# Optimization experiments

Hardware: AMD Instinct MI355X
Metric: run time of the kernel (lower is better)

The kernel has to match this reference:

```python
import jax, jax.numpy as jnp
import numpy as np

B, T, D_IN, D_H1, D_H2, K = 8, 1024, 256, 1024, 1024, 9
EPS = 1e-12

def setup_inputs() -> dict:
    key = jax.random.key(0)
    ks = jax.random.split(key, 11)
    return {
        "x": jax.random.normal(ks[0], (B, T, D_IN), jnp.float32),
        "d_w": jax.random.normal(ks[1], (B, D_H1, 1, K), jnp.float32),
        "d_g": jax.random.uniform(ks[2], (B, D_H1), jnp.float32),
        "d_b": jax.random.normal(ks[3], (B, D_H1), jnp.float32) * 0.02,
        "p_w": jax.random.normal(ks[4], (B, D_H1, D_H2, 1), jnp.float32),
        "p_g": jax.random.uniform(ks[5], (B, D_H1), jnp.float32),
        "p_b": jax.random.normal(ks[6], (B, D_H2), jnp.float32) * 0.02,
        "w1_w": jax.random.normal(ks[7], (D_H1, D_IN), jnp.float32) / np.sqrt(D_IN),
        "w1_b": jnp.zeros((D_H1,), jnp.float32),
        "w2_w": jax.random.normal(ks[8], (D_IN, D_H2), jnp.float32) / np.sqrt(D_H2),
        "w2_b": jnp.zeros((D_IN,), jnp.float32),
    }

def _mish(v):
    return v * jnp.tanh(jax.nn.softplus(v))

def _wnorm(w, g):
    # F.normalize over channel dim 1, scaled by per-(batch,channel) gain g
    n = jnp.maximum(jnp.linalg.norm(w, axis=1, keepdims=True), EPS)
    return (w / n) * g[:, :, None, None]

def reference(x, d_w, d_g, d_b, p_w, p_g, p_b, w1_w, w1_b, w2_w, w2_b):
    residual = x
    # w_1: conv1x1 projection d_in -> d_hid1, channels-first [B, C, T]
    h = jnp.einsum('bti,ci->bct', x, w1_w) + w1_b[None, :, None]
    h = _mish(h)  # dropout is identity in eval
    k = d_w.shape[-1]
    p = (k - 1) // 2
    t = h.shape[-1]
    hp = jnp.pad(h, ((0, 0), (0, 0), (p, p)))
    # unfold: overlapping windows [B, C, T, K] (small fixed K loop)
    x_unf = jnp.stack([hp[:, :, i:i + t] for i in range(k)], axis=-1)
    dw = _wnorm(d_w, d_g)[:, :, 0, :]  # [B, C, K]
    y = jnp.einsum('bctk,bck->bct', x_unf, dw) + d_b[:, :, None]
    pw = _wnorm(p_w, p_g)[..., 0]      # [B, C, O]
    y = jnp.einsum('bct,bco->bot', y, pw) + p_b[:, :, None]
    # w_2: conv1x1 projection d_hid2 -> d_in, back to [B, T, d_in]
    out = jnp.einsum('bot,io->bti', y, w2_w) + w2_b
    return out + residual
```

## Files before the change

kernel.cpp:

```cpp
#include <hip/hip_runtime.h>
#include <hip/hip_bf16.h>

#define B_  8
#define T_  1024
#define DI_ 256
#define C_  1024
#define O_  1024
#define KW  9
#define BT_ 8192
#define EPSF 1e-12f

typedef unsigned short u16;
typedef u16   ushort8 __attribute__((ext_vector_type(8)));
typedef u16   ushort4v __attribute__((ext_vector_type(4)));
typedef __bf16 bf16x8 __attribute__((ext_vector_type(8)));
typedef float  f32x4  __attribute__((ext_vector_type(4)));

#define GLOAD_LDS16(g, l) __builtin_amdgcn_global_load_lds( \
    (const __attribute__((address_space(1))) void*)(g),      \
    (__attribute__((address_space(3))) void*)(l), 16, 0, 0)

__device__ __forceinline__ float bf2f(u16 u) {
    union { unsigned int i; float f; } z; z.i = ((unsigned int)u) << 16; return z.f;
}
__device__ __forceinline__ u16 f2bf(float f) {
    union { float f; unsigned int i; } z; z.f = f;
    unsigned int i = z.i;
    i += 0x7FFFu + ((i >> 16) & 1u);
    return (u16)(i >> 16);
}
__device__ __forceinline__ float mishf(float v) {
    float u = __expf(v);
    float w = 1.f + u;
    return v * (1.f - 2.f / (w * w + 1.f));
}

#define PB_XB 2048
#define PB_W1 2304
#define PB_W2 2560
#define PB_DN 2568
#define PB_PT 4616

__global__ __launch_bounds__(256)
void prep_k(const float* __restrict__ x,   u16* __restrict__ xb,
            const float* __restrict__ w1w, u16* __restrict__ w1b16,
            const float* __restrict__ w2w, u16* __restrict__ w2b16,
            const float* __restrict__ d_w, const float* __restrict__ d_g,
            float* __restrict__ dwf,
            const float* __restrict__ p_w, const float* __restrict__ p_g,
            float* __restrict__ part, u16* __restrict__ pwT)
{
    const int bid = blockIdx.x;
    const int tid = threadIdx.x;

    if (bid < PB_W2) {
        const float* in;
        u16* out;
        int i;
        if (bid < PB_XB)      { in = x;   out = xb;    i = bid * 256 + tid; }
        else if (bid < PB_W1) { in = w1w; out = w1b16; i = (bid - PB_XB) * 256 + tid; }
        else                  { in = w2w; out = w2b16; i = (bid - PB_W1) * 256 + tid; }
        float4 v = ((const float4*)in)[i];
        ushort4v o;
        o.x = f2bf(v.x); o.y = f2bf(v.y); o.z = f2bf(v.z); o.w = f2bf(v.w);
        ((ushort4v*)out)[i] = o;
    } else if (bid < PB_DN) {
        __shared__ float red[KW][256];
        __shared__ float nrm[KW];
        const int b = bid - PB_W2;
        float s[KW];
#pragma unroll
        for (int k = 0; k < KW; k++) s[k] = 0.f;
        for (int c = tid; c < C_; c += 256) {
#pragma unroll
            for (int k = 0; k < KW; k++) {
                float v = d_w[((size_t)b * C_ + c) * KW + k];
                s[k] += v * v;
            }
        }
#pragma unroll
        for (int k = 0; k < KW; k++) red[k][tid] = s[k];
        __syncthreads();
        if (tid < KW) {
            float t = 0.f;
            for (int i = 0; i < 256; i++) t += red[tid][i];
            nrm[tid] = fmaxf(sqrtf(t), EPSF);
        }
        __syncthreads();
        for (int c = tid; c < C_; c += 256) {
            float g = d_g[(size_t)b * C_ + c];
#pragma unroll
            for (int k = 0; k < KW; k++)
                dwf[((size_t)b * C_ + c) * KW + k] =
                    d_w[((size_t)b * C_ + c) * KW + k] / nrm[k] * g;
        }
    } else {
        __shared__ float ts[64][65];
        __shared__ float sq[4][64];
        const int idx = bid - PB_DN;
        const int b   = idx >> 8;
        const int rem = idx & 255;
        const int c0  = (rem >> 4) * 64, o0 = (rem & 15) * 64;
        const int col = tid & 63;
        const int rg  = tid >> 6;
        float ssq = 0.f;
        for (int r = rg; r < 64; r += 4) {
            float v = p_w[((size_t)b * C_ + c0 + r) * O_ + o0 + col];
            ssq += v * v;
            ts[r][col] = v * p_g[(size_t)b * C_ + c0 + r];
        }
        sq[rg][col] = ssq;
        __syncthreads();
        if (tid < 64)
            part[((size_t)b * 16 + (rem >> 4)) * O_ + o0 + tid] =
                sq[0][tid] + sq[1][tid] + sq[2][tid] + sq[3][tid];
        for (int r = rg; r < 64; r += 4)
            pwT[((size_t)b * O_ + o0 + r) * C_ + c0 + col] = f2bf(ts[col][r]);
    }
}

__global__ __launch_bounds__(256)
void dwconv_k(const u16* __restrict__ h, const float* __restrict__ dwf,
              const float* __restrict__ d_b, u16* __restrict__ y1gT)
{
    __shared__ u16 hs[64][74];
    const int b  = blockIdx.z;
    const int c0 = blockIdx.y * 64, t0 = blockIdx.x * 64;
    const int tid = threadIdx.x;
    for (int idx = tid; idx < 64 * 72; idx += 256) {
        int cc = idx / 72, tt = idx % 72;
        int t = t0 + tt - 4;
        u16 v = 0;
        if (t >= 0 && t < T_) v = h[(size_t)(c0 + cc) * BT_ + b * T_ + t];
        hs[cc][tt] = v;
    }
    __syncthreads();
    const int cc = tid & 63;
    const int c  = c0 + cc;
    float w[KW];
#pragma unroll
    for (int k = 0; k < KW; k++) w[k] = dwf[((size_t)b * C_ + c) * KW + k];
    const float bb = d_b[(size_t)b * C_ + c];
    for (int tt = tid >> 6; tt < 64; tt += 4) {
        float s = bb;
#pragma unroll
        for (int k = 0; k < KW; k++) s += bf2f(hs[cc][tt + k]) * w[k];
        y1gT[((size_t)b * T_ + t0 + tt) * C_ + c] = f2bf(s);
    }
}

template<int EPI>
__device__ __forceinline__ void gemm12_body(
    const u16* __restrict__ A, const u16* __restrict__ Bt,
    u16* __restrict__ Db, const float* __restrict__ bias,
    const float* __restrict__ extra, int M, int N, int Kd)
{
    __shared__ u16 As[3 * 128 * 64];
    __shared__ u16 Bs[3 * 256 * 64];

    const int gx = gridDim.x;
    const unsigned nwg = (unsigned)gx * gridDim.y;
    unsigned lin = blockIdx.y * gx + blockIdx.x;
    lin = (lin & 7u) * (nwg >> 3) + (lin >> 3);
    const int m0 = (int)(lin / gx) * 128;
    const int n0 = (int)(lin % gx) * 256;

    const int b = (EPI == 1) ? (m0 >> 10) : 0;
    if (EPI == 1) {
        Bt    += (size_t)b * O_ * C_;
        bias  += (size_t)b * O_;
        extra += (size_t)b * 16 * O_;
    }

    const int tid  = threadIdx.x;
    const int lane = tid & 63, wave = tid >> 6;
    const int wm = (wave >> 2) * 64, wn = (wave & 3) * 64;
    const int lr = lane & 15;
    const int srow8 = tid >> 3;
    const int scolE = ((tid & 7) ^ ((tid >> 3) & 7)) * 8;

    f32x4 acc[4][4];
#pragma unroll
    for (int i = 0; i < 4; i++)
#pragma unroll
        for (int j = 0; j < 4; j++) acc[i][j] = (f32x4){0.f, 0.f, 0.f, 0.f};

    auto STAGE = [&](int buf, int kt) {
        const int k0 = kt << 6;
#pragma unroll
        for (int i = 0; i < 2; i++)
            GLOAD_LDS16(&A[(size_t)(m0 + i * 64 + srow8) * Kd + k0 + scolE],
                        &As[buf * 8192 + (i * 64 + wave * 8) * 64]);
#pragma unroll
        for (int i = 0; i < 4; i++)
            GLOAD_LDS16(&Bt[(size_t)(n0 + i * 64 + srow8) * Kd + k0 + scolE],
                        &Bs[buf * 16384 + (i * 64 + wave * 8) * 64]);
    };

    const int NT = Kd >> 6;
    STAGE(0, 0);
    STAGE(1, 1);
    int rb = 0, sb = 2;
    for (int kt = 0; kt < NT; kt++) {
        if (kt == NT - 1) {
            asm volatile("s_waitcnt vmcnt(0)" ::: "memory");
        } else {
            asm volatile("s_waitcnt vmcnt(6)" ::: "memory");
        }
        __builtin_amdgcn_s_barrier();
        if (kt + 2 < NT) STAGE(sb, kt + 2);
        const u16* as = &As[rb * 8192];
        const u16* bs = &Bs[rb * 16384];
        bf16x8 av[2][4], bv[2][4];
#pragma unroll
        for (int kk = 0; kk < 2; kk++) {
            const int q  = (lane >> 4) + kk * 4;
            const int sw = (q ^ (lr & 7)) << 3;
#pragma unroll
            for (int i = 0; i < 4; i++)
                av[kk][i] = *(const bf16x8*)&as[(wm + i * 16 + lr) * 64 + sw];
#pragma unroll
            for (int j = 0; j < 4; j++)
                bv[kk][j] = *(const bf16x8*)&bs[(wn + j * 16 + lr) * 64 + sw];
        }
        __builtin_amdgcn_s_setprio(1);
#pragma unroll
        for (int kk = 0; kk < 2; kk++)
#pragma unroll
            for (int i = 0; i < 4; i++)
#pragma unroll
                for (int j = 0; j < 4; j++)
                    acc[i][j] = __builtin_amdgcn_mfma_f32_16x16x32_bf16(
                        av[kk][i], bv[kk][j], acc[i][j], 0, 0, 0);
        __builtin_amdgcn_s_setprio(0);
        rb = (rb == 2) ? 0 : rb + 1;
        sb = (sb == 2) ? 0 : sb + 1;
    }

    const int r0 = (lane >> 4) * 4;
#pragma unroll
    for (int i = 0; i < 4; i++) {
#pragma unroll
        for (int j = 0; j < 4; j++) {
            const int col = n0 + wn + j * 16 + lr;
            float iv = 0.f;
            if (EPI == 1) {
                float s = 0.f;
#pragma unroll
                for (int ch = 0; ch < 16; ch++)
                    s += extra[(size_t)ch * O_ + col];
                iv = 1.f / fmaxf(sqrtf(s), EPSF);
            }
#pragma unroll
            for (int r = 0; r < 4; r++) {
                const int row = m0 + wm + i * 16 + r0 + r;
                float v = acc[i][j][r];
                if (EPI == 0) {
                    v += bias[row];
                    v = mishf(v);
                } else {
                    v = v * iv + bias[col];
                }
                Db[(size_t)row * N + col] = f2bf(v);
            }
        }
    }
}

__global__ __launch_bounds__(512, 2)
void gemm1_k(const u16* __restrict__ A, const u16* __restrict__ Bt,
             u16* __restrict__ D, const float* __restrict__ bias,
             int M, int N, int Kd)
{
    gemm12_body<0>(A, Bt, D, bias, nullptr, M, N, Kd);
}

__global__ __launch_bounds__(512, 2)
void gemm2_k(const u16* __restrict__ A, const u16* __restrict__ Bt,
             u16* __restrict__ D, const float* __restrict__ bias,
             const float* __restrict__ extra, int M, int N, int Kd)
{
    gemm12_body<1>(A, Bt, D, bias, extra, M, N, Kd);
}

__global__ __launch_bounds__(128, 2)
void gemm3_k(const u16* __restrict__ A, const u16* __restrict__ Bt,
             float* __restrict__ Df, const float* __restrict__ bias,
             const float* __restrict__ X, int M, int N, int Kd)
{
    __shared__ u16 As[3 * 2048];
    __shared__ u16 Bs[3 * 2048];

    const int gx = gridDim.x;
    const unsigned nwg = (unsigned)gx * gridDim.y;
    unsigned lin = blockIdx.y * gx + blockIdx.x;
    lin = (lin & 7u) * (nwg >> 3) + (lin >> 3);
    const int m0 = (int)(lin / gx) * 64;
    const int n0 = (int)(lin % gx) * 64;

    const int tid  = threadIdx.x;
    const int lane = tid & 63, wave = tid >> 6;
    const int wn = wave * 32;
    const int lr = lane & 15;
    const int q  = lane >> 4;
    const int srow  = lane >> 2;
    const int scolE = ((lane & 3) ^ ((lane >> 3) & 3)) * 8;
    const int sw    = (q ^ ((lr >> 1) & 3)) << 3;

    f32x4 acc[4][2];
#pragma unroll
    for (int i = 0; i < 4; i++)
#pragma unroll
        for (int j = 0; j < 2; j++) acc[i][j] = (f32x4){0.f, 0.f, 0.f, 0.f};

    auto STAGE = [&](int buf, int kt) {
        const int k0 = kt << 5;
#pragma unroll
        for (int i = 0; i < 2; i++)
            GLOAD_LDS16(&A[(size_t)(m0 + wave * 32 + i * 16 + srow) * Kd + k0 + scolE],
                        &As[buf * 2048 + (wave * 32 + i * 16) * 32]);
#pragma unroll
        for (int i = 0; i < 2; i++)
            GLOAD_LDS16(&Bt[(size_t)(n0 + wave * 32 + i * 16 + srow) * Kd + k0 + scolE],
                        &Bs[buf * 2048 + (wave * 32 + i * 16) * 32]);
    };

    const int NT = Kd >> 5;
    STAGE(0, 0);
    STAGE(1, 1);
    int rb = 0, sb = 2;
    for (int kt = 0; kt < NT; kt++) {
        if (kt == NT - 1) {
            asm volatile("s_waitcnt vmcnt(0)" ::: "memory");
        } else {
            asm volatile("s_waitcnt vmcnt(4)" ::: "memory");
        }
        __builtin_amdgcn_s_barrier();
        if (kt + 2 < NT) STAGE(sb, kt + 2);
        const u16* as = &As[rb * 2048];
        const u16* bs = &Bs[rb * 2048];
        bf16x8 av[4], bv[2];
#pragma unroll
        for (int i = 0; i < 4; i++)
            av[i] = *(const bf16x8*)&as[(i * 16 + lr) * 32 + sw];
#pragma unroll
        for (int j = 0; j < 2; j++)
            bv[j] = *(const bf16x8*)&bs[(wn + j * 16 + lr) * 32 + sw];
        __builtin_amdgcn_s_setprio(1);
#pragma unroll
        for (int i = 0; i < 4; i++)
#pragma unroll
            for (int j = 0; j < 2; j++)
                acc[i][j] = __builtin_amdgcn_mfma_f32_16x16x32_bf16(
                    av[i], bv[j], acc[i][j], 0, 0, 0);
        __builtin_amdgcn_s_setprio(0);
        rb = (rb == 2) ? 0 : rb + 1;
        sb = (sb == 2) ? 0 : sb + 1;
    }

    const int r0 = (lane >> 4) * 4;
#pragma unroll
    for (int i = 0; i < 4; i++) {
#pragma unroll
        for (int j = 0; j < 2; j++) {
            const int col = n0 + wn + j * 16 + lr;
#pragma unroll
            for (int r = 0; r < 4; r++) {
                const int row = m0 + i * 16 + r0 + r;
                Df[(size_t)row * N + col] =
                    acc[i][j][r] + bias[col] + X[(size_t)row * N + col];
            }
        }
    }
}

extern "C" void kernel_launch(void* const* d_in, const int* in_sizes, int n_in,
                              void* d_out, int out_size, void* d_ws, size_t ws_size,
                              hipStream_t stream)
{
    const float* x   = (const float*)d_in[0];
    const float* d_w = (const float*)d_in[1];
    const float* d_g = (const float*)d_in[2];
    const float* d_b = (const float*)d_in[3];
    const float* p_w = (const float*)d_in[4];
    const float* p_g = (const float*)d_in[5];
    const float* p_b = (const float*)d_in[6];
    const float* w1w = (const float*)d_in[7];
    const float* w1b = (const float*)d_in[8];
    const float* w2w = (const float*)d_in[9];
    const float* w2b = (const float*)d_in[10];
    float* out = (float*)d_out;

    char* ws = (char*)d_ws;
    const size_t SZ = (size_t)16777216;
    u16*   h    = (u16*)(ws);
    u16*   y1gT = (u16*)(ws + SZ);
    u16*   pwT  = (u16*)(ws + 2 * SZ);
    u16*   y2T  = (u16*)(ws + 3 * SZ);
    u16*   xb   = (u16*)(ws + 4 * SZ);
    u16*   w1b16= (u16*)(ws + 4 * SZ + 4194304);
    u16*   w2b16= (u16*)(ws + 4 * SZ + 4718592);
    float* dwf  = (float*)(ws + 4 * SZ + 5242880);
    float* part = (float*)(ws + 4 * SZ + 5242880 + 294912);

    prep_k<<<dim3(PB_PT), 256, 0, stream>>>(
        x, xb, w1w, w1b16, w2w, w2b16, d_w, d_g, dwf, p_w, p_g, part, pwT);

    gemm1_k<<<dim3(BT_ / 256, C_ / 128), 512, 0, stream>>>(
        w1b16, xb, h, w1b, C_, BT_, DI_);

    dwconv_k<<<dim3(T_ / 64, C_ / 64, B_), 256, 0, stream>>>(h, dwf, d_b, y1gT);

    gemm2_k<<<dim3(O_ / 256, BT_ / 128), 512, 0, stream>>>(
        y1gT, pwT, y2T, p_b, part, BT_, O_, C_);

    gemm3_k<<<dim3(DI_ / 64, BT_ / 64), 128, 0, stream>>>(
        y2T, w2b16, out, w2b, x, BT_, DI_, O_);
}
```

Baseline: 104.0 us.

## Fold pointwise and output projections into one per-batch weight matrix

Uses associativity to combine the per-batch pointwise conv weights (with their column normalization) and the final w2 projection into one [DI x C] matrix per batch, computed by a small batched GEMM. The token-sized GEMM over C->O->DI becomes a single C->DI GEMM, and the p_b bias is folded into a per-batch output bias. This removes the large intermediate y2 and most of the second big GEMM's FLOPs. The cost is an extra weight-only GEMM and an added bf16 rounding of the combined weights, which may shift numerics.

```diff
diff --git a/kernel.cpp b/kernel.cpp
--- a/kernel.cpp
+++ b/kernel.cpp
@@ -37,29 +37,29 @@
 
 #define PB_XB 2048
 #define PB_W1 2304
-#define PB_W2 2560
-#define PB_DN 2568
-#define PB_PT 4616
+#define PB_DN 2312
+#define PB_PW 2824
+#define PB_TOT 2832
 
 __global__ __launch_bounds__(256)
 void prep_k(const float* __restrict__ x,   u16* __restrict__ xb,
             const float* __restrict__ w1w, u16* __restrict__ w1b16,
-            const float* __restrict__ w2w, u16* __restrict__ w2b16,
             const float* __restrict__ d_w, const float* __restrict__ d_g,
             float* __restrict__ dwf,
             const float* __restrict__ p_w, const float* __restrict__ p_g,
-            float* __restrict__ part, u16* __restrict__ pwT)
+            u16* __restrict__ pwb, float* __restrict__ part,
+            const float* __restrict__ w2w, const float* __restrict__ p_b,
+            float* __restrict__ pb2)
 {
     const int bid = blockIdx.x;
     const int tid = threadIdx.x;
 
-    if (bid < PB_W2) {
+    if (bid < PB_W1) {
         const float* in;
         u16* out;
         int i;
-        if (bid < PB_XB)      { in = x;   out = xb;    i = bid * 256 + tid; }
-        else if (bid < PB_W1) { in = w1w; out = w1b16; i = (bid - PB_XB) * 256 + tid; }
-        else                  { in = w2w; out = w2b16; i = (bid - PB_W1) * 256 + tid; }
+        if (bid < PB_XB) { in = x;   out = xb;    i = bid * 256 + tid; }
+        else             { in = w1w; out = w1b16; i = (bid - PB_XB) * 256 + tid; }
         float4 v = ((const float4*)in)[i];
         ushort4v o;
         o.x = f2bf(v.x); o.y = f2bf(v.y); o.z = f2bf(v.z); o.w = f2bf(v.w);
@@ -67,7 +67,7 @@
     } else if (bid < PB_DN) {
         __shared__ float red[KW][256];
         __shared__ float nrm[KW];
-        const int b = bid - PB_W2;
+        const int b = bid - PB_W1;
         float s[KW];
 #pragma unroll
         for (int k = 0; k < KW; k++) s[k] = 0.f;
@@ -94,28 +94,54 @@
                 dwf[((size_t)b * C_ + c) * KW + k] =
                     d_w[((size_t)b * C_ + c) * KW + k] / nrm[k] * g;
         }
+    } else if (bid < PB_PW) {
+        const int idx = bid - PB_DN;
+        const int b   = idx >> 6;
+        const int rem = idx & 63;
+        const int cch = rem >> 2;
+        const int o   = (rem & 3) * 256 + tid;
+        float ssq = 0.f;
+#pragma unroll 8
+        for (int r = 0; r < 64; r++) {
+            const size_t row = (size_t)b * C_ + cch * 64 + r;
+            float v = p_w[row * O_ + o];
+            ssq += v * v;
+            pwb[row * O_ + o] = f2bf(v * p_g[row]);
+        }
+        part[((size_t)b * 16 + cch) * O_ + o] = ssq;
     } else {
-        __shared__ float ts[64][65];
-        __shared__ float sq[4][64];
-        const int idx = bid - PB_DN;
-        const int b   = idx >> 8;
-        const int rem = idx & 255;
-        const int c0  = (rem >> 4) * 64, o0 = (rem & 15) * 64;
-        const int col = tid & 63;
-        const int rg  = tid >> 6;
-        float ssq = 0.f;
-        for (int r = rg; r < 64; r += 4) {
-            float v = p_w[((size_t)b * C_ + c0 + r) * O_ + o0 + col];
-            ssq += v * v;
-            ts[r][col] = v * p_g[(size_t)b * C_ + c0 + r];
-        }
-        sq[rg][col] = ssq;
+        __shared__ float pbs[O_];
+        const int b = bid - PB_PW;
+        for (int j = tid; j < O_; j += 256) pbs[j] = p_b[(size_t)b * O_ + j];
         __syncthreads();
-        if (tid < 64)
-            part[((size_t)b * 16 + (rem >> 4)) * O_ + o0 + tid] =
-                sq[0][tid] + sq[1][tid] + sq[2][tid] + sq[3][tid];
-        for (int r = rg; r < 64; r += 4)
-            pwT[((size_t)b * O_ + o0 + r) * C_ + c0 + col] = f2bf(ts[col][r]);
+        const int i = tid;
+        float s = 0.f;
+        for (int o = 0; o < O_; o += 4) {
+            float4 w = *(const float4*)&w2w[(size_t)i * O_ + o];
+            s += w.x * pbs[o] + w.y * pbs[o + 1] + w.z * pbs[o + 2] + w.w * pbs[o + 3];
+        }
+        pb2[b * DI_ + i] = s;
+    }
+}
+
+__global__ __launch_bounds__(256)
+void w2s_k(const float* __restrict__ w2w, const float* __restrict__ part,
+           u16* __restrict__ w2s)
+{
+    const int bid = blockIdx.x;
+    const int tid = threadIdx.x;
+    const int b   = bid >> 4;
+    const int ich = (bid >> 2) & 3;
+    const int o   = (bid & 3) * 256 + tid;
+    float s = 0.f;
+#pragma unroll
+    for (int ch = 0; ch < 16; ch++)
+        s += part[((size_t)b * 16 + ch) * O_ + o];
+    const float inv = 1.f / fmaxf(sqrtf(s), EPSF);
+#pragma unroll 8
+    for (int r = 0; r < 64; r++) {
+        const int i = ich * 64 + r;
+        w2s[((size_t)b * DI_ + i) * O_ + o] = f2bf(w2w[(size_t)i * O_ + o] * inv);
     }
 }
 
@@ -150,10 +176,10 @@
 }
 
 template<int EPI>
-__device__ __forceinline__ void gemm12_body(
+__device__ __forceinline__ void bgemm_body(
     const u16* __restrict__ A, const u16* __restrict__ Bt,
     u16* __restrict__ Db, const float* __restrict__ bias,
-    const float* __restrict__ extra, int M, int N, int Kd)
+    int N, int Kd)
 {
     __shared__ u16 As[3 * 128 * 64];
     __shared__ u16 Bs[3 * 256 * 64];
@@ -164,13 +190,6 @@
     lin = (lin & 7u) * (nwg >> 3) + (lin >> 3);
     const int m0 = (int)(lin / gx) * 128;
     const int n0 = (int)(lin % gx) * 256;
-
-    const int b = (EPI == 1) ? (m0 >> 10) : 0;
-    if (EPI == 1) {
-        Bt    += (size_t)b * O_ * C_;
-        bias  += (size_t)b * O_;
-        extra += (size_t)b * 16 * O_;
-    }
 
     const int tid  = threadIdx.x;
     const int lane = tid & 63, wave = tid >> 6;
@@ -243,24 +262,11 @@
 #pragma unroll
         for (int j = 0; j < 4; j++) {
             const int col = n0 + wn + j * 16 + lr;
-            float iv = 0.f;
-            if (EPI == 1) {
-                float s = 0.f;
-#pragma unroll
-                for (int ch = 0; ch < 16; ch++)
-                    s += extra[(size_t)ch * O_ + col];
-                iv = 1.f / fmaxf(sqrtf(s), EPSF);
-            }
 #pragma unroll
             for (int r = 0; r < 4; r++) {
                 const int row = m0 + wm + i * 16 + r0 + r;
                 float v = acc[i][j][r];
-                if (EPI == 0) {
-                    v += bias[row];
-                    v = mishf(v);
-                } else {
-                    v = v * iv + bias[col];
-                }
+                if (EPI == 0) v = mishf(v + bias[row]);
                 Db[(size_t)row * N + col] = f2bf(v);
             }
         }
@@ -270,48 +276,52 @@
 __global__ __launch_bounds__(512, 2)
 void gemm1_k(const u16* __restrict__ A, const u16* __restrict__ Bt,
              u16* __restrict__ D, const float* __restrict__ bias,
-             int M, int N, int Kd)
-{
-    gemm12_body<0>(A, Bt, D, bias, nullptr, M, N, Kd);
+             int N, int Kd)
+{
+    bgemm_body<0>(A, Bt, D, bias, N, Kd);
 }
 
 __global__ __launch_bounds__(512, 2)
-void gemm2_k(const u16* __restrict__ A, const u16* __restrict__ Bt,
-             u16* __restrict__ D, const float* __restrict__ bias,
-             const float* __restrict__ extra, int M, int N, int Kd)
-{
-    gemm12_body<1>(A, Bt, D, bias, extra, M, N, Kd);
+void m2_k(const u16* __restrict__ A, const u16* __restrict__ Bt,
+          u16* __restrict__ D)
+{
+    const int b = blockIdx.z;
+    bgemm_body<3>(A + (size_t)b * DI_ * O_, Bt + (size_t)b * C_ * O_,
+                  D + (size_t)b * DI_ * C_, nullptr, C_, O_);
 }
 
 __global__ __launch_bounds__(128, 2)
-void gemm3_k(const u16* __restrict__ A, const u16* __restrict__ Bt,
+void fgemm_k(const u16* __restrict__ A, const u16* __restrict__ Bt,
              float* __restrict__ Df, const float* __restrict__ bias,
-             const float* __restrict__ X, int M, int N, int Kd)
+             const float* __restrict__ pb2, const float* __restrict__ X)
 {
     __shared__ u16 As[3 * 2048];
-    __shared__ u16 Bs[3 * 2048];
+    __shared__ u16 Bs[3 * 4096];
+    const int N = DI_, Kd = C_;
 
     const int gx = gridDim.x;
     const unsigned nwg = (unsigned)gx * gridDim.y;
     unsigned lin = blockIdx.y * gx + blockIdx.x;
     lin = (lin & 7u) * (nwg >> 3) + (lin >> 3);
     const int m0 = (int)(lin / gx) * 64;
-    const int n0 = (int)(lin % gx) * 64;
+    const int n0 = (int)(lin % gx) * 128;
+    const int b  = m0 >> 10;
+    const u16* Bb = Bt + (size_t)b * DI_ * C_;
 
     const int tid  = threadIdx.x;
     const int lane = tid & 63, wave = tid >> 6;
-    const int wn = wave * 32;
+    const int wn = wave * 64;
     const int lr = lane & 15;
     const int q  = lane >> 4;
     const int srow  = lane >> 2;
     const int scolE = ((lane & 3) ^ ((lane >> 3) & 3)) * 8;
     const int sw    = (q ^ ((lr >> 1) & 3)) << 3;
 
-    f32x4 acc[4][2];
+    f32x4 acc[4][4];
 #pragma unroll
     for (int i = 0; i < 4; i++)
 #pragma unroll
-        for (int j = 0; j < 2; j++) acc[i][j] = (f32x4){0.f, 0.f, 0.f, 0.f};
+        for (int j = 0; j < 4; j++) acc[i][j] = (f32x4){0.f, 0.f, 0.f, 0.f};
 
     auto STAGE = [&](int buf, int kt) {
         const int k0 = kt << 5;
@@ -320,9 +330,9 @@
             GLOAD_LDS16(&A[(size_t)(m0 + wave * 32 + i * 16 + srow) * Kd + k0 + scolE],
                         &As[buf * 2048 + (wave * 32 + i * 16) * 32]);
 #pragma unroll
-        for (int i = 0; i < 2; i++)
-            GLOAD_LDS16(&Bt[(size_t)(n0 + wave * 32 + i * 16 + srow) * Kd + k0 + scolE],
-                        &Bs[buf * 2048 + (wave * 32 + i * 16) * 32]);
+        for (int i = 0; i < 4; i++)
+            GLOAD_LDS16(&Bb[(size_t)(n0 + wave * 64 + i * 16 + srow) * Kd + k0 + scolE],
+                        &Bs[buf * 4096 + (wave * 64 + i * 16) * 32]);
     };
 
     const int NT = Kd >> 5;
@@ -333,24 +343,24 @@
         if (kt == NT - 1) {
             asm volatile("s_waitcnt vmcnt(0)" ::: "memory");
         } else {
-            asm volatile("s_waitcnt vmcnt(4)" ::: "memory");
+            asm volatile("s_waitcnt vmcnt(6)" ::: "memory");
         }
         __builtin_amdgcn_s_barrier();
         if (kt + 2 < NT) STAGE(sb, kt + 2);
         const u16* as = &As[rb * 2048];
-        const u16* bs = &Bs[rb * 2048];
-        bf16x8 av[4], bv[2];
+        const u16* bs = &Bs[rb * 4096];
+        bf16x8 av[4], bv[4];
 #pragma unroll
         for (int i = 0; i < 4; i++)
             av[i] = *(const bf16x8*)&as[(i * 16 + lr) * 32 + sw];
 #pragma unroll
-        for (int j = 0; j < 2; j++)
+        for (int j = 0; j < 4; j++)
             bv[j] = *(const bf16x8*)&bs[(wn + j * 16 + lr) * 32 + sw];
         __builtin_amdgcn_s_setprio(1);
 #pragma unroll
         for (int i = 0; i < 4; i++)
 #pragma unroll
-            for (int j = 0; j < 2; j++)
+            for (int j = 0; j < 4; j++)
                 acc[i][j] = __builtin_amdgcn_mfma_f32_16x16x32_bf16(
                     av[i], bv[j], acc[i][j], 0, 0, 0);
         __builtin_amdgcn_s_setprio(0);
@@ -362,13 +372,14 @@
 #pragma unroll
     for (int i = 0; i < 4; i++) {
 #pragma unroll
-        for (int j = 0; j < 2; j++) {
+        for (int j = 0; j < 4; j++) {
             const int col = n0 + wn + j * 16 + lr;
+            const float cadd = bias[col] + pb2[b * DI_ + col];
 #pragma unroll
             for (int r = 0; r < 4; r++) {
                 const int row = m0 + i * 16 + r0 + r;
                 Df[(size_t)row * N + col] =
-                    acc[i][j][r] + bias[col] + X[(size_t)row * N + col];
+                    acc[i][j][r] + cadd + X[(size_t)row * N + col];
             }
         }
     }
@@ -395,25 +406,27 @@
     const size_t SZ = (size_t)16777216;
     u16*   h    = (u16*)(ws);
     u16*   y1gT = (u16*)(ws + SZ);
-    u16*   pwT  = (u16*)(ws + 2 * SZ);
-    u16*   y2T  = (u16*)(ws + 3 * SZ);
-    u16*   xb   = (u16*)(ws + 4 * SZ);
-    u16*   w1b16= (u16*)(ws + 4 * SZ + 4194304);
-    u16*   w2b16= (u16*)(ws + 4 * SZ + 4718592);
-    float* dwf  = (float*)(ws + 4 * SZ + 5242880);
-    float* part = (float*)(ws + 4 * SZ + 5242880 + 294912);
-
-    prep_k<<<dim3(PB_PT), 256, 0, stream>>>(
-        x, xb, w1w, w1b16, w2w, w2b16, d_w, d_g, dwf, p_w, p_g, part, pwT);
+    u16*   pwb  = (u16*)(ws + 2 * SZ);
+    u16*   xb   = (u16*)(ws + 3 * SZ);
+    u16*   w1b16= (u16*)(ws + 3 * SZ + 4194304);
+    u16*   w2s  = (u16*)(ws + 3 * SZ + 4718592);
+    u16*   M2   = (u16*)(ws + 3 * SZ + 8912896);
+    float* dwf  = (float*)(ws + 3 * SZ + 13107200);
+    float* part = (float*)(ws + 3 * SZ + 13402112);
+    float* pb2  = (float*)(ws + 3 * SZ + 13926400);
+
+    prep_k<<<dim3(PB_TOT), 256, 0, stream>>>(
+        x, xb, w1w, w1b16, d_w, d_g, dwf, p_w, p_g, pwb, part, w2w, p_b, pb2);
+
+    w2s_k<<<dim3(128), 256, 0, stream>>>(w2w, part, w2s);
 
     gemm1_k<<<dim3(BT_ / 256, C_ / 128), 512, 0, stream>>>(
-        w1b16, xb, h, w1b, C_, BT_, DI_);
+        w1b16, xb, h, w1b, BT_, DI_);
 
     dwconv_k<<<dim3(T_ / 64, C_ / 64, B_), 256, 0, stream>>>(h, dwf, d_b, y1gT);
 
-    gemm2_k<<<dim3(O_ / 256, BT_ / 128), 512, 0, stream>>>(
-        y1gT, pwT, y2T, p_b, part, BT_, O_, C_);
-
-    gemm3_k<<<dim3(DI_ / 64, BT_ / 64), 128, 0, stream>>>(
-        y2T, w2b16, out, w2b, x, BT_, DI_, O_);
-}
+    m2_k<<<dim3(C_ / 256, DI_ / 128, B_), 512, 0, stream>>>(w2s, pwb, M2);
+
+    fgemm_k<<<dim3(DI_ / 128, BT_ / 64), 128, 0, stream>>>(
+        y1gT, M2, out, w2b, pb2, x);
+}
```

Result: slower. 130.3 us (+25.3%).
